# Kernel optimization log

Hardware: AMD Instinct MI355X
Metric: run time of the kernel (lower is better)

Reference implementation:

```python
import jax, jax.numpy as jnp
import numpy as np

B, NEG = 2, 16            # queries, negatives per query
N, E, D = 10000, 80000, 128  # nodes, edges, feature dim (in_dim == out_dim)
NUM_REL = 237
L = 3                     # PNA layers
NODE_RATIO = 0.1
K = max(1, int(NODE_RATIO * N))  # static top-k: every repeated graph has exactly N nodes
EPS = 1e-5


def _score(hidden, rel, lin_W, lin_b, m1_W, m1_b, m2_W, m2_b):
    heur = jnp.concatenate([hidden, rel], axis=-1) @ lin_W + lin_b
    x = heur * hidden
    h = jax.nn.relu(x @ m1_W + m1_b)
    return jnp.squeeze(h @ m2_W + m2_b, -1)


def _pna_conv(hidden, src, dst, emask, deg, pre_W, pre_b, post_W, post_b, out_W, out_b):
    """PNA layer with mean/max/min/std aggregators and identity/amplification/attenuation
    scalers, restricted to edges where emask is True. deg is the (clamped >=1) degree used
    by the scalers."""
    BN = hidden.shape[0]
    # message: pre-linear on [x_i (target), x_j (source)] per edge  -> (Erep, D)
    m = jnp.concatenate([hidden[dst], hidden[src]], axis=-1) @ pre_W + pre_b
    w = emask.astype(hidden.dtype)[:, None]
    cnt = jax.ops.segment_sum(emask.astype(hidden.dtype), dst, num_segments=BN)
    denom = jnp.maximum(cnt, 1.0)[:, None]
    s1 = jax.ops.segment_sum(m * w, dst, num_segments=BN)
    s2 = jax.ops.segment_sum(m * m * w, dst, num_segments=BN)
    mean = s1 / denom
    var = jax.nn.relu(s2 / denom - mean * mean)
    std = jnp.sqrt(var + EPS)
    has = (cnt > 0)[:, None]
    mx = jnp.where(has, jax.ops.segment_max(jnp.where(emask[:, None], m, -jnp.inf), dst, num_segments=BN), 0.0)
    mn = jnp.where(has, jax.ops.segment_min(jnp.where(emask[:, None], m, jnp.inf), dst, num_segments=BN), 0.0)
    agg = jnp.concatenate([mean, mx, mn, std], axis=-1)           # (BN, 4D)
    logd = jnp.log(deg + 1.0)                                     # deg >= 1 -> logd > 0
    avg_log = jnp.mean(logd)
    agg = jnp.concatenate([agg, agg * (logd / avg_log)[:, None], agg * (avg_log / logd)[:, None]], axis=-1)  # (BN, 12D)
    return (agg @ post_W + post_b) @ out_W + out_b


def _forward(h_index, r_index, t_index, hidden_states, edge_index, rel_embedding,
             lin_W, lin_b, m1_W, m1_b, m2_W, m2_b, pre_W, pre_b, post_W, post_b, out_W, out_b):
    sc = (lin_W, lin_b, m1_W, m1_b, m2_W, m2_b)
    # negative_sample_to_tail
    is_t_neg = jnp.all(h_index == h_index[:, :1], axis=-1, keepdims=True)
    h_idx = jnp.where(is_t_neg, h_index, t_index)
    t_idx = jnp.where(is_t_neg, t_index, h_index)
    r_idx = jnp.where(is_t_neg, r_index, r_index + NUM_REL)
    # repeat_graph
    offsets = jnp.arange(B, dtype=h_idx.dtype) * N               # (B,)
    src = jnp.tile(edge_index[0], B) + jnp.repeat(offsets, E)    # (B*E,)
    dst = jnp.tile(edge_index[1], B) + jnp.repeat(offsets, E)
    BN = B * N
    rel_embeds = rel_embedding[r_idx[:, 0]].astype(hidden_states.dtype)  # (B, D)
    flat_h = h_idx[:, 0] + offsets
    flat_t = t_idx[:, 0] + offsets
    # literal `repeat_interleave(N, dim=0)[:B]` quirk -> row arange(B)//N of gathered embs
    sel = jnp.arange(B) // N
    h_vals = hidden_states[h_idx[:, 0]][sel]                     # (B, D)
    t_vals = hidden_states[t_idx[:, 0]][sel]
    # init_input_embeds: boundary condition + initial score at head nodes
    boundary = jnp.zeros((BN, D), hidden_states.dtype).at[flat_t].set(t_vals).at[flat_h].set(h_vals)
    score = jnp.zeros(BN, jnp.float32).at[flat_h].set(_score(h_vals, rel_embeds, *sc))
    hidden = boundary
    rel_per_node = jnp.repeat(rel_embeds, N, axis=0)             # (BN, D), rel_embeds[batch_rep]
    rows = jnp.arange(B)[:, None]
    for l in range(L):
        # select_edges_pyg with degree_ratio=1.0: all out-edges of per-graph top-k nodes
        _, idx = jax.lax.top_k(score.reshape(B, N), K)           # (B, K)
        node_sel = jnp.zeros((B, N), bool).at[rows, idx].set(True).reshape(-1)
        emask = node_sel[src]                                    # (B*E,) selected-edge mask
        out_deg = jax.ops.segment_sum(emask.astype(jnp.float32), src, num_segments=BN)
        deg_sub = jnp.maximum(out_deg.astype(hidden.dtype), 1.0)
        new_hidden = _pna_conv(hidden, src, dst, emask, deg_sub,
                               pre_W[l], pre_b[l], post_W[l], post_b[l], out_W[l], out_b[l])
        # residual only for nodes with selected outgoing edges
        hidden = jnp.where((out_deg > 0)[:, None], hidden + new_hidden, hidden)
        score = _score(hidden, rel_per_node, *sc)
    # read out scores at (repeated) tail indices -> (B, NEG)
    return score[t_idx + offsets[:, None]]


def setup_inputs() -> dict:
    key = jax.random.key(0)
    ks = jax.random.split(key, 14)
    s = 0.05
    hi = jax.random.randint(ks[0], (B, 1), 0, N)
    h_index = jnp.tile(hi, (1, NEG))                 # constant per row (assert in forward)
    r0 = jax.random.randint(ks[1], (B, 1), 0, NUM_REL)
    r_index = jnp.tile(r0, (1, NEG))                 # constant per row (assert in forward)
    t_index = jax.random.randint(ks[2], (B, NEG), 0, N)
    hidden_states = jax.random.normal(ks[3], (N, D), jnp.float32)
    edge_index = jax.random.randint(ks[4], (2, E), 0, N)
    return {
        "h_index": h_index, "r_index": r_index, "t_index": t_index,
        "hidden_states": hidden_states, "edge_index": edge_index,
        "rel_embedding": jax.random.normal(ks[5], (2 * NUM_REL, D), jnp.float32) * s,
        "lin_W": jax.random.normal(ks[6], (2 * D, D), jnp.float32) * s, "lin_b": jnp.zeros(D, jnp.float32),
        "m1_W": jax.random.normal(ks[7], (D, D), jnp.float32) * s, "m1_b": jnp.zeros(D, jnp.float32),
        "m2_W": jax.random.normal(ks[8], (D, 1), jnp.float32) * s, "m2_b": jnp.zeros(1, jnp.float32),
        "pre_W": jax.random.normal(ks[9], (L, 2 * D, D), jnp.float32) * s, "pre_b": jnp.zeros((L, D), jnp.float32),
        "post_W": jax.random.normal(ks[10], (L, 12 * D, D), jnp.float32) * s, "post_b": jnp.zeros((L, D), jnp.float32),
        "out_W": jax.random.normal(ks[11], (L, D, D), jnp.float32) * s, "out_b": jnp.zeros((L, D), jnp.float32),
    }


def reference(h_index, r_index, t_index, hidden_states, edge_index, rel_embedding,
              lin_W, lin_b, m1_W, m1_b, m2_W, m2_b, pre_W, pre_b, post_W, post_b, out_W, out_b):
    return _forward(h_index, r_index, t_index, hidden_states, edge_index, rel_embedding,
                    lin_W, lin_b, m1_W, m1_b, m2_W, m2_b, pre_W, pre_b, post_W, post_b, out_W, out_b)
```

## Files before the change

### kernel.cpp

```cpp
#include <hip/hip_runtime.h>
#include <math.h>

#define Bq 2
#define NEG 16
#define Nn 10000
#define Ee 80000
#define Dd 128
#define NUM_REL 237
#define Ll 3
#define K_SEL 1000
#define BN (Bq*Nn)
#define EPSV 1e-5f
#define MAXACT 2048
#define MAXTOUCH 8192
#define SELCAP 3328
#define LN2F 0.69314718056f

constexpr size_t HID_OFF   = 0;
constexpr size_t SCORE_OFF = HID_OFF   + (size_t)BN*Dd*4;
constexpr size_t CVEC_OFF  = SCORE_OFF + (size_t)BN*4;
constexpr size_t HDR_OFF   = CVEC_OFF  + (size_t)Bq*Dd*4;
constexpr size_t THR_OFF   = HDR_OFF   + 64*4;
constexpr size_t SEL_OFF   = THR_OFF   + Bq*8;
constexpr size_t DEG_OFF   = SEL_OFF   + (size_t)BN*4;
constexpr size_t SLOT_OFF  = DEG_OFF   + (size_t)BN*4;
constexpr size_t CNT_OFF   = SLOT_OFF  + (size_t)BN*4;
constexpr size_t SDEG_OFF  = CNT_OFF   + (size_t)MAXACT*4;
constexpr size_t S1_OFF    = SDEG_OFF  + (size_t)MAXACT*4;
constexpr size_t S2_OFF    = S1_OFF    + (size_t)MAXACT*Dd*4;
constexpr size_t MXB_OFF   = S2_OFF    + (size_t)MAXACT*Dd*4;
constexpr size_t MNB_OFF   = MXB_OFF   + (size_t)MAXACT*Dd*4;
constexpr size_t TPART_OFF = MNB_OFF   + (size_t)MAXACT*Dd*4;
constexpr size_t ALIST_OFF = TPART_OFF + (size_t)4*MAXACT*Dd*4;
constexpr size_t FLAG_OFF  = ALIST_OFF + (size_t)MAXACT*4;
constexpr size_t TLIST_OFF = FLAG_OFF  + (size_t)BN*4;
constexpr size_t EDGE_OFF  = TLIST_OFF + (size_t)MAXTOUCH*4;
constexpr size_t CTR_OFF   = EDGE_OFF  + (size_t)Bq*Ee*2*4;

__device__ __forceinline__ unsigned encf(float f){
  unsigned u = __float_as_uint(f);
  return (u & 0x80000000u) ? ~u : (u | 0x80000000u);
}
__device__ __forceinline__ float decf(unsigned e){
  unsigned u = (e & 0x80000000u) ? (e & 0x7FFFFFFFu) : ~e;
  return __uint_as_float(u);
}
__device__ __forceinline__ unsigned long long make_key(float f, int i){
  unsigned d = ~encf(f);
  return ((unsigned long long)d << 32) | (unsigned)i;
}

__global__ void k_zero(float* hidden, unsigned* flag){
  int i = blockIdx.x*blockDim.x + threadIdx.x;
  if (i < BN*Dd/4) ((float4*)hidden)[i] = make_float4(0.f,0.f,0.f,0.f);
  if (i < BN) flag[i] = 0u;
}

__global__ __launch_bounds__(256) void k_prep(
    const int* h_index, const int* r_index, const int* t_index,
    const float* hidden_states, const float* rel_embedding,
    const float* lin_W, const float* lin_b, const float* m1_W, const float* m1_b,
    const float* m2_W, const float* m2_b,
    int* hdr, float* cvec, float* hidden, float* score,
    unsigned* flag, int* tlist, unsigned* ctr){
  __shared__ int sh_fh[Bq], sh_ft[Bq], sh_r0[Bq], sh_hsrc, sh_tsrc;
  __shared__ float s_relv[Bq][Dd], s_cvec[Bq][Dd], s_hv[Dd], s_x[Bq][Dd], s_p[Bq][Dd];
  __shared__ float s_s0[Dd];
  __shared__ float sc0_sh;
  int tid = threadIdx.x;
  if (tid == 0){
    int n = 0;
    for (int b=0;b<Bq;b++){
      bool eq = true;
      for (int j=1;j<NEG;j++) eq = eq && (h_index[b*NEG+j]==h_index[b*NEG]);
      int h0 = eq ? h_index[b*NEG] : t_index[b*NEG];
      int t0 = eq ? t_index[b*NEG] : h_index[b*NEG];
      int r0 = eq ? r_index[b*NEG] : r_index[b*NEG] + NUM_REL;
      sh_fh[b] = h0 + b*Nn; sh_ft[b] = t0 + b*Nn; sh_r0[b] = r0;
      hdr[0+b] = sh_fh[b]; hdr[2+b] = sh_ft[b];
      for (int j=0;j<NEG;j++){
        int tj = eq ? t_index[b*NEG+j] : h_index[b*NEG+j];
        hdr[4 + b*NEG + j] = tj + b*Nn;
      }
      if (b==0){ sh_hsrc = h0; sh_tsrc = t0; }
      if (!flag[sh_ft[b]]){ flag[sh_ft[b]] = 1u; tlist[n++] = sh_ft[b]; }
      if (!flag[sh_fh[b]]){ flag[sh_fh[b]] = 1u; tlist[n++] = sh_fh[b]; }
    }
    ctr[3] = (unsigned)n;
  }
  __syncthreads();
  int b = tid >> 7, d = tid & 127;
  s_relv[b][d] = rel_embedding[(size_t)sh_r0[b]*Dd + d];
  if (b == 0){
    s_hv[d] = hidden_states[(size_t)sh_hsrc*Dd + d];
    s_s0[d] = fmaxf(m1_b[d], 0.f) * m2_W[d];
  }
  __syncthreads();
  if (tid == 0){
    float s = m2_b[0];
    for (int k=0;k<Dd;k++) s += s_s0[k];
    sc0_sh = s;
    ctr[4] = __float_as_uint(s);
  }
  float acc = lin_b[d];
  #pragma unroll 8
  for (int k=0;k<Dd;k++) acc += s_relv[b][k]*lin_W[(Dd+k)*Dd + d];
  s_cvec[b][d] = acc; cvec[b*Dd+d] = acc;
  hidden[(size_t)sh_ft[b]*Dd + d] = hidden_states[(size_t)sh_tsrc*Dd + d];
  hidden[(size_t)sh_fh[b]*Dd + d] = hidden_states[(size_t)sh_hsrc*Dd + d];
  __syncthreads();
  float sc0 = sc0_sh;
  for (int i = tid; i < BN; i += 256) score[i] = sc0;
  float hv = s_hv[d];
  float heur = s_cvec[b][d];
  #pragma unroll 8
  for (int k=0;k<Dd;k++) heur += s_hv[k]*lin_W[k*Dd + d];
  s_x[b][d] = heur * hv;
  __syncthreads();
  float a2 = m1_b[d];
  #pragma unroll 8
  for (int k=0;k<Dd;k++) a2 += s_x[b][k]*m1_W[k*Dd + d];
  s_p[b][d] = fmaxf(a2, 0.f) * m2_W[d];
  __syncthreads();
  if (tid < Bq){
    float s = m2_b[0];
    for (int k=0;k<Dd;k++) s += s_p[tid][k];
    score[sh_fh[tid]] = s;
  }
}

__global__ __launch_bounds__(256) void k_select(
    const float* score, const int* tlist, const unsigned* ctr,
    unsigned long long* thr){
  int b = blockIdx.x;
  int nt = (int)ctr[3];
  unsigned d0 = ~encf(__uint_as_float(ctr[4]));
  __shared__ unsigned sd[SELCAP];
  __shared__ unsigned short sidx[SELCAP];
  __shared__ unsigned hist[256], histT[256];
  __shared__ int ntb_sh;
  __shared__ unsigned long long pref_sh;
  __shared__ unsigned kk_sh;
  int tid = threadIdx.x;
  if (tid==0){ ntb_sh = 0; pref_sh = 0ull; kk_sh = K_SEL; }
  __syncthreads();
  int vlo = b*Nn, vhi = vlo + Nn;
  for (int i = tid; i < nt; i += 256){
    int v = tlist[i];
    if (v >= vlo && v < vhi){
      int pos = atomicAdd(&ntb_sh, 1);
      if (pos < SELCAP){
        sd[pos] = ~encf(score[v]);
        sidx[pos] = (unsigned short)(v - vlo);
      }
    }
  }
  __syncthreads();
  int ntb = min(ntb_sh, SELCAP);
  unsigned nvirt = (unsigned)(Nn - ntb);
  for (int pass = 7; pass >= 0; --pass){
    hist[tid] = 0u; histT[tid] = 0u;
    __syncthreads();
    unsigned long long pref = pref_sh;
    int sh_hi = 8*(pass+1);
    for (int j = tid; j < ntb; j += 256){
      unsigned long long key = ((unsigned long long)sd[j] << 32) | (unsigned long long)sidx[j];
      bool ok = (pass==7) || ((key >> sh_hi) == (pref >> sh_hi));
      if (ok) atomicAdd(&hist[(unsigned)(key >> (8*pass)) & 255u], 1u);
      if (pass < 4){
        unsigned idx = sidx[j];
        bool oki = (pass == 3) || ((idx >> sh_hi) == (((unsigned)pref) >> sh_hi));
        if (oki) atomicAdd(&histT[(idx >> (8*pass)) & 255u], 1u);
      }
    }
    __syncthreads();
    if (pass >= 4){
      if (tid == 0){
        unsigned long long keyv_hi = ((unsigned long long)d0 << 32);
        bool ok = (pass==7) || ((keyv_hi >> sh_hi) == (pref >> sh_hi));
        if (ok) atomicAdd(&hist[(d0 >> (8*(pass-4))) & 255u], nvirt);
      }
    } else {
      if ((unsigned)(pref >> 32) == d0){
        unsigned long long hf = 0ull;
        if (pass < 3) hf = (unsigned long long)((((unsigned)pref) >> sh_hi)) << sh_hi;
        unsigned long long lo = hf + ((unsigned long long)tid << (8*pass));
        unsigned long long hi = lo + (1ull << (8*pass));
        unsigned long long nn = (unsigned long long)Nn;
        unsigned long long l2 = lo < nn ? lo : nn;
        unsigned long long h2 = hi < nn ? hi : nn;
        if (h2 > l2){
          unsigned c = (unsigned)(h2 - l2) - histT[tid];
          if (c > 0u) atomicAdd(&hist[tid], c);
        }
      }
    }
    __syncthreads();
    if (tid < 256){
      unsigned kk = kk_sh;
      unsigned cum = 0;
      for (int i=0;i<tid;i++) cum += hist[i];
      unsigned h = hist[tid];
      if (h > 0u && cum < kk && kk <= cum + h){
        pref_sh |= ((unsigned long long)tid) << (8*pass);
        kk_sh = kk - cum;
      }
    }
    __syncthreads();
  }
  if (tid==0) thr[b] = pref_sh;
}

__global__ void k_mask(const float* score, const unsigned long long* thr, unsigned* sel,
                       unsigned* out_deg, float* s1, float* s2,
                       unsigned* mxb, unsigned* mnb, unsigned* cnt, unsigned* ctr){
  int i = blockIdx.x*blockDim.x + threadIdx.x;
  if (i < BN){
    int b = i / Nn; int v = i - b*Nn;
    sel[i] = (make_key(score[i], v) <= thr[b]) ? 1u : 0u;
    out_deg[i] = 0u;
  }
  if (i < MAXACT*Dd){ s1[i]=0.f; s2[i]=0.f; mxb[i]=0u; mnb[i]=0xFFFFFFFFu; }
  if (i < MAXACT) cnt[i]=0u;
  if (i < 3) ctr[i]=0u;
}

__global__ void k_degree(const int* ei, const unsigned* sel, unsigned* out_deg){
  int e = blockIdx.x*blockDim.x + threadIdx.x;
  if (e >= Ee) return;
  int s0 = ei[e];
  #pragma unroll
  for (int b=0;b<Bq;b++){
    int v = s0 + b*Nn;
    if (sel[v]) atomicAdd(&out_deg[v], 1u);
  }
}

__global__ void k_active(const unsigned* out_deg, int* node_slot, int* alist,
                         float* slot_deg, unsigned* ctr, unsigned* flag, int* tlist){
  int v = blockIdx.x*blockDim.x + threadIdx.x;
  if (v >= BN) return;
  unsigned dg = out_deg[v];
  if (dg > 0u){
    int slot = (int)atomicAdd(&ctr[0], 1u);
    alist[slot] = v; node_slot[v] = slot; slot_deg[slot] = (float)dg;
    atomicAdd((float*)&ctr[2], logf((float)dg + 1.0f));
    if (atomicExch(&flag[v], 1u) == 0u){
      int p = (int)atomicAdd(&ctr[3], 1u);
      tlist[p] = v;
    }
  }
}

__global__ void k_edges(const int* ei, const unsigned* sel, const unsigned* out_deg,
                        const int* node_slot, int* edges, unsigned* cnt, unsigned* ctr){
  int e = blockIdx.x*blockDim.x + threadIdx.x;
  if (e >= Ee) return;
  int s0 = ei[e], d0 = ei[Ee + e];
  #pragma unroll
  for (int b=0;b<Bq;b++){
    int s = s0 + b*Nn, dv = d0 + b*Nn;
    if (sel[s] && out_deg[dv] > 0u){
      int slot = node_slot[dv];
      int j = (int)atomicAdd(&ctr[1], 1u);
      edges[2*j] = s; edges[2*j+1] = slot;
      atomicAdd(&cnt[slot], 1u);
    }
  }
}

__global__ __launch_bounds__(128) void k_messages(
    const float* hidden, const int* edges, const int* alist,
    const float* preW, const float* preb,
    float* s1, float* s2, unsigned* mxb, unsigned* mnb, const unsigned* ctr){
  int ne = (int)ctr[1];
  int tid = threadIdx.x;
  __shared__ float sd[4][Dd], ss[4][Dd];
  __shared__ int dsl[4];
  float pb = preb[tid];
  for (int j0 = blockIdx.x*4; j0 < ne; j0 += gridDim.x*4){
    int nv = ne - j0; if (nv > 4) nv = 4;
    if (tid < 4){
      int j = j0 + ((tid < nv) ? tid : 0);
      dsl[tid] = edges[2*j+1];
    }
    #pragma unroll
    for (int e=0;e<4;e++){
      int j = j0 + ((e < nv) ? e : 0);
      int s = edges[2*j];
      int dv = alist[edges[2*j+1]];
      sd[e][tid] = hidden[(size_t)dv*Dd + tid];
      ss[e][tid] = hidden[(size_t)s*Dd + tid];
    }
    __syncthreads();
    float a[4] = {pb, pb, pb, pb};
    #pragma unroll 4
    for (int k=0;k<Dd;k++){
      float w0 = preW[k*Dd + tid];
      float w1 = preW[(Dd+k)*Dd + tid];
      #pragma unroll
      for (int e=0;e<4;e++) a[e] += sd[e][k]*w0 + ss[e][k]*w1;
    }
    for (int e=0;e<nv;e++){
      int dslot = dsl[e];
      atomicAdd(&s1[dslot*Dd + tid], a[e]);
      atomicAdd(&s2[dslot*Dd + tid], a[e]*a[e]);
      atomicMax(&mxb[dslot*Dd + tid], encf(a[e]));
      atomicMin(&mnb[dslot*Dd + tid], encf(a[e]));
    }
    __syncthreads();
  }
}

__global__ __launch_bounds__(512) void k_post(
    const unsigned* cnt, const float* s1, const float* s2,
    const unsigned* mxb, const unsigned* mnb, const float* slot_deg,
    const float* postW, float* tpart, const unsigned* ctr){
  int na = (int)ctr[0];
  int bid = blockIdx.x;
  int tile = bid & 63, ch = bid >> 6;
  if (tile*32 >= na) return;
  float logsum = __uint_as_float(ctr[2]);
  float avg = (logsum + (float)(BN - na)*LN2F) / (float)BN;
  __shared__ float lb[32*136];
  __shared__ float wbuf[3*16*128];
  __shared__ float sden[32];
  __shared__ unsigned shas[32];
  int tid = threadIdx.x;
  if (tid < 32){
    unsigned c = cnt[tile*32 + tid];
    sden[tid] = fmaxf((float)c, 1.0f);
    shas[tid] = c;
  }
  __syncthreads();
  for (int idx = tid; idx < 32*Dd; idx += 512){
    int sl = idx >> 7, kk = idx & 127;
    int gi = (tile*32 + sl)*Dd + kk;
    float den = sden[sl];
    float val;
    if (ch == 0)      val = s1[gi]/den;
    else if (ch == 1) val = shas[sl] ? decf(mxb[gi]) : 0.f;
    else if (ch == 2) val = shas[sl] ? decf(mnb[gi]) : 0.f;
    else {
      float mv = s1[gi]/den;
      float var = s2[gi]/den - mv*mv;
      val = sqrtf(fmaxf(var, 0.f) + EPSV);
    }
    lb[sl*136 + kk] = val;
  }
  int cg = tid & 31, rg = tid >> 5;
  int c0 = cg*4;
  float a0[2][4], a1[2][4], a2[2][4];
  #pragma unroll
  for (int i=0;i<2;i++)
    #pragma unroll
    for (int j=0;j<4;j++){ a0[i][j]=0.f; a1[i][j]=0.f; a2[i][j]=0.f; }
  for (int chunk = 0; chunk < 8; ++chunk){
    #pragma unroll
    for (int i = 0; i < 3; ++i){
      int f = tid + i*512;
      int q = f >> 9, r = f & 511;
      int kk = r >> 5, c4 = r & 31;
      int grow = q*512 + ch*128 + chunk*16 + kk;
      ((float4*)wbuf)[f] = *(const float4*)(postW + (size_t)grow*Dd + c4*4);
    }
    __syncthreads();
    #pragma unroll
    for (int k4 = 0; k4 < 4; ++k4){
      float4 av0 = *(const float4*)&lb[(rg*2+0)*136 + chunk*16 + k4*4];
      float4 av1 = *(const float4*)&lb[(rg*2+1)*136 + chunk*16 + k4*4];
      #pragma unroll
      for (int j = 0; j < 4; ++j){
        int kk = k4*4 + j;
        float4 w0 = *(const float4*)&wbuf[kk*128 + c0];
        float4 w1 = *(const float4*)&wbuf[(16+kk)*128 + c0];
        float4 w2 = *(const float4*)&wbuf[(32+kk)*128 + c0];
        float av[2] = { (&av0.x)[j], (&av1.x)[j] };
        #pragma unroll
        for (int i=0;i<2;i++){
          float a = av[i];
          a0[i][0] += a*w0.x; a0[i][1] += a*w0.y; a0[i][2] += a*w0.z; a0[i][3] += a*w0.w;
          a1[i][0] += a*w1.x; a1[i][1] += a*w1.y; a1[i][2] += a*w1.z; a1[i][3] += a*w1.w;
          a2[i][0] += a*w2.x; a2[i][1] += a*w2.y; a2[i][2] += a*w2.z; a2[i][3] += a*w2.w;
        }
      }
    }
    __syncthreads();
  }
  #pragma unroll
  for (int i=0;i<2;i++){
    int slot = tile*32 + rg*2 + i;
    if (slot < na){
      float dg = slot_deg[slot];
      float logd = logf(dg + 1.f);
      float al = logd/avg, be = avg/logd;
      float4 r;
      r.x = a0[i][0] + al*a1[i][0] + be*a2[i][0];
      r.y = a0[i][1] + al*a1[i][1] + be*a2[i][1];
      r.z = a0[i][2] + al*a1[i][2] + be*a2[i][2];
      r.w = a0[i][3] + al*a1[i][3] + be*a2[i][3];
      *(float4*)(tpart + (size_t)ch*MAXACT*Dd + (size_t)slot*Dd + c0) = r;
    }
  }
}

__global__ __launch_bounds__(256) void k_out_resid(
    const float* tpart, const int* alist, const float* outW, const float* outb,
    const float* postb, float* hidden, const unsigned* ctr){
  int na = (int)ctr[0];
  int tile = blockIdx.x;
  if (tile*32 >= na) return;
  __shared__ float tr[32*136];
  __shared__ float wbuf[16*128];
  int tid = threadIdx.x;
  for (int idx = tid; idx < 32*Dd; idx += 256){
    int sl = idx >> 7, kk = idx & 127;
    size_t o = (size_t)(tile*32 + sl)*Dd + kk;
    tr[sl*136 + kk] = tpart[o] + tpart[(size_t)MAXACT*Dd + o]
                    + tpart[(size_t)2*MAXACT*Dd + o] + tpart[(size_t)3*MAXACT*Dd + o]
                    + postb[kk];
  }
  int cg = tid & 31, rg = tid >> 5;
  int c0 = cg*4;
  float4 ob = *(const float4*)(outb + c0);
  float acc[4][4];
  #pragma unroll
  for (int r=0;r<4;r++){ acc[r][0]=ob.x; acc[r][1]=ob.y; acc[r][2]=ob.z; acc[r][3]=ob.w; }
  for (int chunk = 0; chunk < 8; ++chunk){
    #pragma unroll
    for (int i = 0; i < 2; ++i){
      int f = tid + i*256;
      int kk = f >> 5, c4 = f & 31;
      ((float4*)wbuf)[f] = *(const float4*)(outW + (size_t)(chunk*16 + kk)*Dd + c4*4);
    }
    __syncthreads();
    #pragma unroll
    for (int k4 = 0; k4 < 4; ++k4){
      float4 av[4];
      #pragma unroll
      for (int r=0;r<4;r++)
        av[r] = *(const float4*)&tr[(rg*4+r)*136 + chunk*16 + k4*4];
      #pragma unroll
      for (int j = 0; j < 4; ++j){
        float4 w = *(const float4*)&wbuf[(k4*4+j)*128 + c0];
        #pragma unroll
        for (int r=0;r<4;r++){
          float a = (&av[r].x)[j];
          acc[r][0] += a*w.x; acc[r][1] += a*w.y; acc[r][2] += a*w.z; acc[r][3] += a*w.w;
        }
      }
    }
    __syncthreads();
  }
  #pragma unroll
  for (int r=0;r<4;r++){
    int slot = tile*32 + rg*4 + r;
    if (slot < na){
      int v = alist[slot];
      float* hp = hidden + (size_t)v*Dd + c0;
      float4 h4 = *(float4*)hp;
      h4.x += acc[r][0]; h4.y += acc[r][1]; h4.z += acc[r][2]; h4.w += acc[r][3];
      *(float4*)hp = h4;
    }
  }
}

__global__ __launch_bounds__(256) void k_score(
    const float* hidden, const float* cvec, const float* linW,
    const float* m1W, const float* m1b, const float* m2W, const float* m2b,
    const int* tlist, const unsigned* ctr, float* score,
    const int* ovr, int ovr_n){
  int nt = (ovr_n > 0) ? ovr_n : (int)ctr[3];
  const int* list = (ovr_n > 0) ? ovr : tlist;
  int nb = blockIdx.x * 32;
  if (nb >= nt) return;
  __shared__ float sh[32*Dd];
  __shared__ float sx[32*Dd];
  __shared__ float sc[2*Dd];
  __shared__ int   sv[32];
  __shared__ float red[32*33];
  int tid = threadIdx.x;
  if (tid < 32){
    int idx = nb + tid;
    sv[tid] = (idx < nt) ? list[idx] : list[nb];
  }
  sc[tid] = cvec[tid];
  __syncthreads();
  for (int q = tid; q < 32*32; q += 256){
    int row = q >> 5, f4 = q & 31;
    ((float4*)sh)[row*32 + f4] = ((const float4*)(hidden + (size_t)sv[row]*Dd))[f4];
  }
  __syncthreads();
  int cg = tid & 31, rg = tid >> 5;
  int c0 = cg*4;
  float acc[4][4];
  #pragma unroll
  for (int i=0;i<4;i++){ acc[i][0]=0.f; acc[i][1]=0.f; acc[i][2]=0.f; acc[i][3]=0.f; }
  for (int k4=0;k4<32;k4++){
    float4 av[4];
    #pragma unroll
    for (int i=0;i<4;i++) av[i] = ((float4*)sh)[(rg*4+i)*32 + k4];
    #pragma unroll
    for (int j=0;j<4;j++){
      float4 w = *(const float4*)(linW + (size_t)(k4*4+j)*Dd + c0);
      #pragma unroll
      for (int i=0;i<4;i++){
        float a = (&av[i].x)[j];
        acc[i][0] += a*w.x; acc[i][1] += a*w.y; acc[i][2] += a*w.z; acc[i][3] += a*w.w;
      }
    }
  }
  #pragma unroll
  for (int i=0;i<4;i++){
    int row = rg*4 + i;
    int bb = (sv[row] >= Nn) ? 1 : 0;
    float4 cv = *(float4*)&sc[bb*Dd + c0];
    float4 hv = ((float4*)sh)[row*32 + cg];
    float4 x;
    x.x = (acc[i][0] + cv.x)*hv.x;
    x.y = (acc[i][1] + cv.y)*hv.y;
    x.z = (acc[i][2] + cv.z)*hv.z;
    x.w = (acc[i][3] + cv.w)*hv.w;
    ((float4*)sx)[row*32 + cg] = x;
  }
  __syncthreads();
  #pragma unroll
  for (int i=0;i<4;i++){ acc[i][0]=0.f; acc[i][1]=0.f; acc[i][2]=0.f; acc[i][3]=0.f; }
  for (int k4=0;k4<32;k4++){
    float4 av[4];
    #pragma unroll
    for (int i=0;i<4;i++) av[i] = ((float4*)sx)[(rg*4+i)*32 + k4];
    #pragma unroll
    for (int j=0;j<4;j++){
      float4 w = *(const float4*)(m1W + (size_t)(k4*4+j)*Dd + c0);
      #pragma unroll
      for (int i=0;i<4;i++){
        float a = (&av[i].x)[j];
        acc[i][0] += a*w.x; acc[i][1] += a*w.y; acc[i][2] += a*w.z; acc[i][3] += a*w.w;
      }
    }
  }
  float4 mb = *(const float4*)(m1b + c0);
  float4 mw = *(const float4*)(m2W + c0);
  #pragma unroll
  for (int i=0;i<4;i++){
    float p0 = fmaxf(acc[i][0]+mb.x, 0.f)*mw.x;
    float p1 = fmaxf(acc[i][1]+mb.y, 0.f)*mw.y;
    float p2 = fmaxf(acc[i][2]+mb.z, 0.f)*mw.z;
    float p3 = fmaxf(acc[i][3]+mb.w, 0.f)*mw.w;
    red[(rg*4+i)*33 + cg] = p0+p1+p2+p3;
  }
  __syncthreads();
  if (tid < 32){
    float s = m2b[0];
    for (int g=0; g<32; g++) s += red[tid*33 + g];
    if (nb + tid < nt) score[sv[tid]] = s;
  }
}

__global__ void k_gather(const float* score, const int* hdr, float* out){
  int i = threadIdx.x;
  if (i < Bq*NEG) out[i] = score[hdr[4+i]];
}

extern "C" void kernel_launch(void* const* d_in, const int* in_sizes, int n_in,
                              void* d_out, int out_size, void* d_ws, size_t ws_size,
                              hipStream_t stream){
  const int*   h_index       = (const int*)d_in[0];
  const int*   r_index       = (const int*)d_in[1];
  const int*   t_index       = (const int*)d_in[2];
  const float* hidden_states = (const float*)d_in[3];
  const int*   edge_index    = (const int*)d_in[4];
  const float* rel_embedding = (const float*)d_in[5];
  const float* lin_W  = (const float*)d_in[6];
  const float* lin_b  = (const float*)d_in[7];
  const float* m1_W   = (const float*)d_in[8];
  const float* m1_b   = (const float*)d_in[9];
  const float* m2_W   = (const float*)d_in[10];
  const float* m2_b   = (const float*)d_in[11];
  const float* pre_W  = (const float*)d_in[12];
  const float* pre_b  = (const float*)d_in[13];
  const float* post_W = (const float*)d_in[14];
  const float* post_b = (const float*)d_in[15];
  const float* out_W  = (const float*)d_in[16];
  const float* out_b  = (const float*)d_in[17];

  char* ws = (char*)d_ws;
  float*    hidden   = (float*)(ws + HID_OFF);
  float*    score    = (float*)(ws + SCORE_OFF);
  float*    cvec     = (float*)(ws + CVEC_OFF);
  int*      hdr      = (int*)(ws + HDR_OFF);
  unsigned long long* thr = (unsigned long long*)(ws + THR_OFF);
  unsigned* sel      = (unsigned*)(ws + SEL_OFF);
  unsigned* out_deg  = (unsigned*)(ws + DEG_OFF);
  int*      node_slot= (int*)(ws + SLOT_OFF);
  unsigned* cnt      = (unsigned*)(ws + CNT_OFF);
  float*    slot_deg = (float*)(ws + SDEG_OFF);
  float*    s1       = (float*)(ws + S1_OFF);
  float*    s2       = (float*)(ws + S2_OFF);
  unsigned* mxb      = (unsigned*)(ws + MXB_OFF);
  unsigned* mnb      = (unsigned*)(ws + MNB_OFF);
  float*    tpart    = (float*)(ws + TPART_OFF);
  int*      alist    = (int*)(ws + ALIST_OFF);
  unsigned* flag     = (unsigned*)(ws + FLAG_OFF);
  int*      tlist    = (int*)(ws + TLIST_OFF);
  int*      edges    = (int*)(ws + EDGE_OFF);
  unsigned* ctr      = (unsigned*)(ws + CTR_OFF);

  k_zero<<<(BN*Dd/4 + 255)/256, 256, 0, stream>>>(hidden, flag);
  k_prep<<<1, 256, 0, stream>>>(h_index, r_index, t_index, hidden_states, rel_embedding,
                                lin_W, lin_b, m1_W, m1_b, m2_W, m2_b,
                                hdr, cvec, hidden, score, flag, tlist, ctr);
  for (int l = 0; l < Ll; ++l){
    const float* preWl  = pre_W  + (size_t)l*2*Dd*Dd;
    const float* prebl  = pre_b  + (size_t)l*Dd;
    const float* postWl = post_W + (size_t)l*12*Dd*Dd;
    const float* postbl = post_b + (size_t)l*Dd;
    const float* outWl  = out_W  + (size_t)l*Dd*Dd;
    const float* outbl  = out_b  + (size_t)l*Dd;

    k_select<<<Bq, 256, 0, stream>>>(score, tlist, ctr, thr);
    k_mask<<<(MAXACT*Dd + 255)/256, 256, 0, stream>>>(score, thr, sel, out_deg,
                                                      s1, s2, mxb, mnb, cnt, ctr);
    k_degree<<<(Ee + 255)/256, 256, 0, stream>>>(edge_index, sel, out_deg);
    k_active<<<(BN + 255)/256, 256, 0, stream>>>(out_deg, node_slot, alist, slot_deg,
                                                 ctr, flag, tlist);
    k_edges<<<(Ee + 255)/256, 256, 0, stream>>>(edge_index, sel, out_deg, node_slot,
                                                edges, cnt, ctr);
    k_messages<<<512, 128, 0, stream>>>(hidden, edges, alist, preWl, prebl,
                                        s1, s2, mxb, mnb, ctr);
    k_post<<<256, 512, 0, stream>>>(cnt, s1, s2, mxb, mnb, slot_deg, postWl, tpart, ctr);
    k_out_resid<<<MAXACT/32, 256, 0, stream>>>(tpart, alist, outWl, outbl, postbl,
                                               hidden, ctr);
    if (l < Ll-1){
      k_score<<<MAXTOUCH/32, 256, 0, stream>>>(hidden, cvec, lin_W, m1_W, m1_b, m2_W, m2_b,
                                               tlist, ctr, score, tlist, 0);
    } else {
      k_score<<<1, 256, 0, stream>>>(hidden, cvec, lin_W, m1_W, m1_b, m2_W, m2_b,
                                     tlist, ctr, score, hdr + 4, Bq*NEG);
    }
  }
  k_gather<<<1, 64, 0, stream>>>(score, hdr, (float*)d_out);
}
```

Before: 481.7 us.

## Fuse init, selection+zeroing, mask into degree, edge filtering into messages

Measured after the change: 538.6 us. +11.8%, slower.

```diff
diff --git a/kernel.cpp b/kernel.cpp
--- a/kernel.cpp
+++ b/kernel.cpp
@@ -21,8 +21,7 @@
 constexpr size_t CVEC_OFF  = SCORE_OFF + (size_t)BN*4;
 constexpr size_t HDR_OFF   = CVEC_OFF  + (size_t)Bq*Dd*4;
 constexpr size_t THR_OFF   = HDR_OFF   + 64*4;
-constexpr size_t SEL_OFF   = THR_OFF   + Bq*8;
-constexpr size_t DEG_OFF   = SEL_OFF   + (size_t)BN*4;
+constexpr size_t DEG_OFF   = THR_OFF   + 64*8;
 constexpr size_t SLOT_OFF  = DEG_OFF   + (size_t)BN*4;
 constexpr size_t CNT_OFF   = SLOT_OFF  + (size_t)BN*4;
 constexpr size_t SDEG_OFF  = CNT_OFF   + (size_t)MAXACT*4;
@@ -50,89 +49,121 @@
   return ((unsigned long long)d << 32) | (unsigned)i;
 }
 
-__global__ void k_zero(float* hidden, unsigned* flag){
-  int i = blockIdx.x*blockDim.x + threadIdx.x;
-  if (i < BN*Dd/4) ((float4*)hidden)[i] = make_float4(0.f,0.f,0.f,0.f);
-  if (i < BN) flag[i] = 0u;
-}
-
-__global__ __launch_bounds__(256) void k_prep(
+__global__ __launch_bounds__(256) void k_init(
     const int* h_index, const int* r_index, const int* t_index,
     const float* hidden_states, const float* rel_embedding,
     const float* lin_W, const float* lin_b, const float* m1_W, const float* m1_b,
     const float* m2_W, const float* m2_b,
     int* hdr, float* cvec, float* hidden, float* score,
     unsigned* flag, int* tlist, unsigned* ctr){
-  __shared__ int sh_fh[Bq], sh_ft[Bq], sh_r0[Bq], sh_hsrc, sh_tsrc;
-  __shared__ float s_relv[Bq][Dd], s_cvec[Bq][Dd], s_hv[Dd], s_x[Bq][Dd], s_p[Bq][Dd];
-  __shared__ float s_s0[Dd];
-  __shared__ float sc0_sh;
+  __shared__ int sfh[Bq], sft[Bq], sr0[Bq], shsrc, stsrc;
+  __shared__ float sp[Dd];
+  __shared__ float ssc0;
+  __shared__ float relv[Bq][Dd], cvv[Bq][Dd], hv[Dd], xx[Bq][Dd], pp[Bq][Dd];
   int tid = threadIdx.x;
   if (tid == 0){
-    int n = 0;
     for (int b=0;b<Bq;b++){
       bool eq = true;
       for (int j=1;j<NEG;j++) eq = eq && (h_index[b*NEG+j]==h_index[b*NEG]);
       int h0 = eq ? h_index[b*NEG] : t_index[b*NEG];
       int t0 = eq ? t_index[b*NEG] : h_index[b*NEG];
       int r0 = eq ? r_index[b*NEG] : r_index[b*NEG] + NUM_REL;
-      sh_fh[b] = h0 + b*Nn; sh_ft[b] = t0 + b*Nn; sh_r0[b] = r0;
-      hdr[0+b] = sh_fh[b]; hdr[2+b] = sh_ft[b];
-      for (int j=0;j<NEG;j++){
-        int tj = eq ? t_index[b*NEG+j] : h_index[b*NEG+j];
-        hdr[4 + b*NEG + j] = tj + b*Nn;
-      }
-      if (b==0){ sh_hsrc = h0; sh_tsrc = t0; }
-      if (!flag[sh_ft[b]]){ flag[sh_ft[b]] = 1u; tlist[n++] = sh_ft[b]; }
-      if (!flag[sh_fh[b]]){ flag[sh_fh[b]] = 1u; tlist[n++] = sh_fh[b]; }
-    }
-    ctr[3] = (unsigned)n;
-  }
-  __syncthreads();
-  int b = tid >> 7, d = tid & 127;
-  s_relv[b][d] = rel_embedding[(size_t)sh_r0[b]*Dd + d];
-  if (b == 0){
-    s_hv[d] = hidden_states[(size_t)sh_hsrc*Dd + d];
-    s_s0[d] = fmaxf(m1_b[d], 0.f) * m2_W[d];
-  }
+      sfh[b] = h0 + b*Nn; sft[b] = t0 + b*Nn; sr0[b] = r0;
+      if (b==0){ shsrc = h0; stsrc = t0; }
+    }
+  }
+  if (tid < Dd) sp[tid] = fmaxf(m1_b[tid], 0.f) * m2_W[tid];
   __syncthreads();
   if (tid == 0){
     float s = m2_b[0];
-    for (int k=0;k<Dd;k++) s += s_s0[k];
-    sc0_sh = s;
-    ctr[4] = __float_as_uint(s);
-  }
-  float acc = lin_b[d];
-  #pragma unroll 8
-  for (int k=0;k<Dd;k++) acc += s_relv[b][k]*lin_W[(Dd+k)*Dd + d];
-  s_cvec[b][d] = acc; cvec[b*Dd+d] = acc;
-  hidden[(size_t)sh_ft[b]*Dd + d] = hidden_states[(size_t)sh_tsrc*Dd + d];
-  hidden[(size_t)sh_fh[b]*Dd + d] = hidden_states[(size_t)sh_hsrc*Dd + d];
-  __syncthreads();
-  float sc0 = sc0_sh;
-  for (int i = tid; i < BN; i += 256) score[i] = sc0;
-  float hv = s_hv[d];
-  float heur = s_cvec[b][d];
-  #pragma unroll 8
-  for (int k=0;k<Dd;k++) heur += s_hv[k]*lin_W[k*Dd + d];
-  s_x[b][d] = heur * hv;
-  __syncthreads();
-  float a2 = m1_b[d];
-  #pragma unroll 8
-  for (int k=0;k<Dd;k++) a2 += s_x[b][k]*m1_W[k*Dd + d];
-  s_p[b][d] = fmaxf(a2, 0.f) * m2_W[d];
-  __syncthreads();
-  if (tid < Bq){
-    float s = m2_b[0];
-    for (int k=0;k<Dd;k++) s += s_p[tid][k];
-    score[sh_fh[tid]] = s;
-  }
-}
-
-__global__ __launch_bounds__(256) void k_select(
-    const float* score, const int* tlist, const unsigned* ctr,
-    unsigned long long* thr){
-  int b = blockIdx.x;
+    for (int k=0;k<Dd;k++) s += sp[k];
+    ssc0 = s;
+  }
+  __syncthreads();
+  float sc0 = ssc0;
+  int fh0 = sfh[0], fh1 = sfh[1], ft0 = sft[0], ft1 = sft[1];
+  int gth = blockIdx.x*256 + tid, gstr = gridDim.x*256;
+  for (int i = gth; i < BN*Dd/4; i += gstr){
+    int row = i >> 5, c4 = i & 31;
+    float4 v;
+    if (row == fh0 || row == fh1)
+      v = ((const float4*)(hidden_states + (size_t)shsrc*Dd))[c4];
+    else if (row == ft0 || row == ft1)
+      v = ((const float4*)(hidden_states + (size_t)stsrc*Dd))[c4];
+    else v = make_float4(0.f,0.f,0.f,0.f);
+    ((float4*)hidden)[i] = v;
+  }
+  for (int i = gth; i < BN; i += gstr){
+    flag[i] = (i==fh0 || i==fh1 || i==ft0 || i==ft1) ? 1u : 0u;
+    if (i != fh0 && i != fh1) score[i] = sc0;
+  }
+  if (blockIdx.x == 0){
+    if (tid == 0){
+      int tl[4]; int n = 0;
+      for (int b=0;b<Bq;b++){
+        hdr[b] = sfh[b]; hdr[2+b] = sft[b];
+        bool eq = true;
+        for (int j=1;j<NEG;j++) eq = eq && (h_index[b*NEG+j]==h_index[b*NEG]);
+        for (int j=0;j<NEG;j++){
+          int tj = eq ? t_index[b*NEG+j] : h_index[b*NEG+j];
+          hdr[4 + b*NEG + j] = tj + b*Nn;
+        }
+        int c1 = sft[b]; bool f1=false;
+        for (int q=0;q<n;q++) f1 = f1 || (tl[q]==c1);
+        if (!f1) tl[n++] = c1;
+        int c2 = sfh[b]; bool f2=false;
+        for (int q=0;q<n;q++) f2 = f2 || (tl[q]==c2);
+        if (!f2) tl[n++] = c2;
+      }
+      for (int q=0;q<n;q++) tlist[q] = tl[q];
+      ctr[3] = (unsigned)n;
+      ctr[4] = __float_as_uint(sc0);
+    }
+    int b = tid >> 7, d = tid & 127;
+    relv[b][d] = rel_embedding[(size_t)sr0[b]*Dd + d];
+    if (b == 0) hv[d] = hidden_states[(size_t)shsrc*Dd + d];
+    __syncthreads();
+    float acc = lin_b[d];
+    #pragma unroll 8
+    for (int k=0;k<Dd;k++) acc += relv[b][k]*lin_W[(Dd+k)*Dd + d];
+    cvv[b][d] = acc; cvec[b*Dd+d] = acc;
+    float heur = acc;
+    #pragma unroll 8
+    for (int k=0;k<Dd;k++) heur += hv[k]*lin_W[k*Dd + d];
+    xx[b][d] = heur * hv[d];
+    __syncthreads();
+    float a2 = m1_b[d];
+    #pragma unroll 8
+    for (int k=0;k<Dd;k++) a2 += xx[b][k]*m1_W[k*Dd + d];
+    pp[b][d] = fmaxf(a2, 0.f) * m2_W[d];
+    __syncthreads();
+    if (tid < Bq){
+      float s = m2_b[0];
+      for (int k=0;k<Dd;k++) s += pp[tid][k];
+      score[sfh[tid]] = s;
+    }
+  }
+}
+
+__global__ __launch_bounds__(256) void k_selz(
+    const float* score, const int* tlist, unsigned* ctr, unsigned long long* thr,
+    unsigned* out_deg, float* s1, float* s2, unsigned* mxb, unsigned* mnb, unsigned* cnt){
+  int bid = blockIdx.x, tid = threadIdx.x;
+  if (bid >= 2){
+    int z0 = (bid-2)*256 + tid, zstr = (gridDim.x-2)*256;
+    float4 z4 = make_float4(0.f,0.f,0.f,0.f);
+    uint4 zi = make_uint4(0u,0u,0u,0u);
+    uint4 fi = make_uint4(~0u,~0u,~0u,~0u);
+    for (int i=z0; i<MAXACT*Dd/4; i+=zstr){
+      ((float4*)s1)[i]=z4; ((float4*)s2)[i]=z4;
+      ((uint4*)mxb)[i]=zi; ((uint4*)mnb)[i]=fi;
+    }
+    for (int i=z0; i<BN; i+=zstr) out_deg[i]=0u;
+    for (int i=z0; i<MAXACT; i+=zstr) cnt[i]=0u;
+    if (bid==2 && tid<3) ctr[tid]=0u;
+    return;
+  }
+  int b = bid;
   int nt = (int)ctr[3];
   unsigned d0 = ~encf(__uint_as_float(ctr[4]));
   __shared__ unsigned sd[SELCAP];
@@ -141,7 +172,6 @@
   __shared__ int ntb_sh;
   __shared__ unsigned long long pref_sh;
   __shared__ unsigned kk_sh;
-  int tid = threadIdx.x;
   if (tid==0){ ntb_sh = 0; pref_sh = 0ull; kk_sh = K_SEL; }
   __syncthreads();
   int vlo = b*Nn, vhi = vlo + Nn;
@@ -211,28 +241,22 @@
   if (tid==0) thr[b] = pref_sh;
 }
 
-__global__ void k_mask(const float* score, const unsigned long long* thr, unsigned* sel,
-                       unsigned* out_deg, float* s1, float* s2,
-                       unsigned* mxb, unsigned* mnb, unsigned* cnt, unsigned* ctr){
-  int i = blockIdx.x*blockDim.x + threadIdx.x;
-  if (i < BN){
-    int b = i / Nn; int v = i - b*Nn;
-    sel[i] = (make_key(score[i], v) <= thr[b]) ? 1u : 0u;
-    out_deg[i] = 0u;
-  }
-  if (i < MAXACT*Dd){ s1[i]=0.f; s2[i]=0.f; mxb[i]=0u; mnb[i]=0xFFFFFFFFu; }
-  if (i < MAXACT) cnt[i]=0u;
-  if (i < 3) ctr[i]=0u;
-}
-
-__global__ void k_degree(const int* ei, const unsigned* sel, unsigned* out_deg){
+__global__ void k_degree(const int* ei, const float* score, const unsigned long long* thr,
+                         unsigned* out_deg, int* sedges, unsigned* ctr){
   int e = blockIdx.x*blockDim.x + threadIdx.x;
   if (e >= Ee) return;
-  int s0 = ei[e];
-  #pragma unroll
-  for (int b=0;b<Bq;b++){
-    int v = s0 + b*Nn;
-    if (sel[v]) atomicAdd(&out_deg[v], 1u);
+  unsigned long long th0 = thr[0], th1 = thr[1];
+  int s0 = ei[e], d0 = ei[Ee + e];
+  if (make_key(score[s0], s0) <= th0){
+    atomicAdd(&out_deg[s0], 1u);
+    int j = (int)atomicAdd(&ctr[1], 1u);
+    sedges[2*j] = s0; sedges[2*j+1] = d0;
+  }
+  int s1v = s0 + Nn, d1v = d0 + Nn;
+  if (make_key(score[s1v], s0) <= th1){
+    atomicAdd(&out_deg[s1v], 1u);
+    int j = (int)atomicAdd(&ctr[1], 1u);
+    sedges[2*j] = s1v; sedges[2*j+1] = d1v;
   }
 }
 
@@ -252,63 +276,64 @@
   }
 }
 
-__global__ void k_edges(const int* ei, const unsigned* sel, const unsigned* out_deg,
-                        const int* node_slot, int* edges, unsigned* cnt, unsigned* ctr){
-  int e = blockIdx.x*blockDim.x + threadIdx.x;
-  if (e >= Ee) return;
-  int s0 = ei[e], d0 = ei[Ee + e];
-  #pragma unroll
-  for (int b=0;b<Bq;b++){
-    int s = s0 + b*Nn, dv = d0 + b*Nn;
-    if (sel[s] && out_deg[dv] > 0u){
-      int slot = node_slot[dv];
-      int j = (int)atomicAdd(&ctr[1], 1u);
-      edges[2*j] = s; edges[2*j+1] = slot;
-      atomicAdd(&cnt[slot], 1u);
-    }
-  }
-}
-
+#define MSG_GRID 512
 __global__ __launch_bounds__(128) void k_messages(
-    const float* hidden, const int* edges, const int* alist,
+    const float* hidden, const int* sedges, const int* node_slot, const unsigned* out_deg,
     const float* preW, const float* preb,
-    float* s1, float* s2, unsigned* mxb, unsigned* mnb, const unsigned* ctr){
-  int ne = (int)ctr[1];
+    float* s1, float* s2, unsigned* mxb, unsigned* mnb, unsigned* cnt, const unsigned* ctr){
+  int ns = (int)ctr[1];
   int tid = threadIdx.x;
-  __shared__ float sd[4][Dd], ss[4][Dd];
+  int bid = blockIdx.x;
+  __shared__ int qs[128], qd[128], qsl[128];
+  __shared__ int qn_sh;
+  __shared__ float sdl[4][Dd], ssl[4][Dd];
   __shared__ int dsl[4];
   float pb = preb[tid];
-  for (int j0 = blockIdx.x*4; j0 < ne; j0 += gridDim.x*4){
-    int nv = ne - j0; if (nv > 4) nv = 4;
-    if (tid < 4){
-      int j = j0 + ((tid < nv) ? tid : 0);
-      dsl[tid] = edges[2*j+1];
-    }
-    #pragma unroll
-    for (int e=0;e<4;e++){
-      int j = j0 + ((e < nv) ? e : 0);
-      int s = edges[2*j];
-      int dv = alist[edges[2*j+1]];
-      sd[e][tid] = hidden[(size_t)dv*Dd + tid];
-      ss[e][tid] = hidden[(size_t)s*Dd + tid];
-    }
-    __syncthreads();
-    float a[4] = {pb, pb, pb, pb};
-    #pragma unroll 4
-    for (int k=0;k<Dd;k++){
-      float w0 = preW[k*Dd + tid];
-      float w1 = preW[(Dd+k)*Dd + tid];
+  int kmax = (ns - bid + MSG_GRID - 1) / MSG_GRID;
+  if (bid >= ns) kmax = 0;
+  for (int k0 = 0; k0 < kmax; k0 += 128){
+    if (tid == 0) qn_sh = 0;
+    __syncthreads();
+    int k = k0 + tid;
+    if (k < kmax){
+      int j = bid + k*MSG_GRID;
+      int dv = sedges[2*j+1];
+      if (out_deg[dv] > 0u){
+        int slot = node_slot[dv];
+        int p = atomicAdd(&qn_sh, 1);
+        qs[p] = sedges[2*j]; qd[p] = dv; qsl[p] = slot;
+        atomicAdd(&cnt[slot], 1u);
+      }
+    }
+    __syncthreads();
+    int nq = qn_sh;
+    for (int q0 = 0; q0 < nq; q0 += 4){
+      int nv = nq - q0; if (nv > 4) nv = 4;
+      if (tid < 4) dsl[tid] = qsl[q0 + ((tid < nv) ? tid : 0)];
       #pragma unroll
-      for (int e=0;e<4;e++) a[e] += sd[e][k]*w0 + ss[e][k]*w1;
-    }
-    for (int e=0;e<nv;e++){
-      int dslot = dsl[e];
-      atomicAdd(&s1[dslot*Dd + tid], a[e]);
-      atomicAdd(&s2[dslot*Dd + tid], a[e]*a[e]);
-      atomicMax(&mxb[dslot*Dd + tid], encf(a[e]));
-      atomicMin(&mnb[dslot*Dd + tid], encf(a[e]));
-    }
-    __syncthreads();
+      for (int e2=0;e2<4;e2++){
+        int qq = q0 + ((e2 < nv) ? e2 : 0);
+        sdl[e2][tid] = hidden[(size_t)qd[qq]*Dd + tid];
+        ssl[e2][tid] = hidden[(size_t)qs[qq]*Dd + tid];
+      }
+      __syncthreads();
+      float a[4] = {pb, pb, pb, pb};
+      #pragma unroll 4
+      for (int kk=0;kk<Dd;kk++){
+        float w0 = preW[kk*Dd + tid];
+        float w1 = preW[(Dd+kk)*Dd + tid];
+        #pragma unroll
+        for (int e2=0;e2<4;e2++) a[e2] += sdl[e2][kk]*w0 + ssl[e2][kk]*w1;
+      }
+      for (int e2=0;e2<nv;e2++){
+        int dslot = dsl[e2];
+        atomicAdd(&s1[dslot*Dd + tid], a[e2]);
+        atomicAdd(&s2[dslot*Dd + tid], a[e2]*a[e2]);
+        atomicMax(&mxb[dslot*Dd + tid], encf(a[e2]));
+        atomicMin(&mnb[dslot*Dd + tid], encf(a[e2]));
+      }
+      __syncthreads();
+    }
   }
 }
 
@@ -469,7 +494,7 @@
     const float* hidden, const float* cvec, const float* linW,
     const float* m1W, const float* m1b, const float* m2W, const float* m2b,
     const int* tlist, const unsigned* ctr, float* score,
-    const int* ovr, int ovr_n){
+    const int* ovr, int ovr_n, float* outdest){
   int nt = (ovr_n > 0) ? ovr_n : (int)ctr[3];
   const int* list = (ovr_n > 0) ? ovr : tlist;
   int nb = blockIdx.x * 32;
@@ -554,13 +579,11 @@
   if (tid < 32){
     float s = m2b[0];
     for (int g=0; g<32; g++) s += red[tid*33 + g];
-    if (nb + tid < nt) score[sv[tid]] = s;
-  }
-}
-
-__global__ void k_gather(const float* score, const int* hdr, float* out){
-  int i = threadIdx.x;
-  if (i < Bq*NEG) out[i] = score[hdr[4+i]];
+    if (nb + tid < nt){
+      if (outdest) outdest[nb + tid] = s;
+      else         score[sv[tid]] = s;
+    }
+  }
 }
 
 extern "C" void kernel_launch(void* const* d_in, const int* in_sizes, int n_in,
@@ -591,7 +614,6 @@
   float*    cvec     = (float*)(ws + CVEC_OFF);
   int*      hdr      = (int*)(ws + HDR_OFF);
   unsigned long long* thr = (unsigned long long*)(ws + THR_OFF);
-  unsigned* sel      = (unsigned*)(ws + SEL_OFF);
   unsigned* out_deg  = (unsigned*)(ws + DEG_OFF);
   int*      node_slot= (int*)(ws + SLOT_OFF);
   unsigned* cnt      = (unsigned*)(ws + CNT_OFF);
@@ -604,13 +626,12 @@
   int*      alist    = (int*)(ws + ALIST_OFF);
   unsigned* flag     = (unsigned*)(ws + FLAG_OFF);
   int*      tlist    = (int*)(ws + TLIST_OFF);
-  int*      edges    = (int*)(ws + EDGE_OFF);
+  int*      sedges   = (int*)(ws + EDGE_OFF);
   unsigned* ctr      = (unsigned*)(ws + CTR_OFF);
 
-  k_zero<<<(BN*Dd/4 + 255)/256, 256, 0, stream>>>(hidden, flag);
-  k_prep<<<1, 256, 0, stream>>>(h_index, r_index, t_index, hidden_states, rel_embedding,
-                                lin_W, lin_b, m1_W, m1_b, m2_W, m2_b,
-                                hdr, cvec, hidden, score, flag, tlist, ctr);
+  k_init<<<2048, 256, 0, stream>>>(h_index, r_index, t_index, hidden_states, rel_embedding,
+                                   lin_W, lin_b, m1_W, m1_b, m2_W, m2_b,
+                                   hdr, cvec, hidden, score, flag, tlist, ctr);
   for (int l = 0; l < Ll; ++l){
     const float* preWl  = pre_W  + (size_t)l*2*Dd*Dd;
     const float* prebl  = pre_b  + (size_t)l*Dd;
@@ -619,26 +640,21 @@
     const float* outWl  = out_W  + (size_t)l*Dd*Dd;
     const float* outbl  = out_b  + (size_t)l*Dd;
 
-    k_select<<<Bq, 256, 0, stream>>>(score, tlist, ctr, thr);
-    k_mask<<<(MAXACT*Dd + 255)/256, 256, 0, stream>>>(score, thr, sel, out_deg,
-                                                      s1, s2, mxb, mnb, cnt, ctr);
-    k_degree<<<(Ee + 255)/256, 256, 0, stream>>>(edge_index, sel, out_deg);
+    k_selz<<<512, 256, 0, stream>>>(score, tlist, ctr, thr, out_deg, s1, s2, mxb, mnb, cnt);
+    k_degree<<<(Ee + 255)/256, 256, 0, stream>>>(edge_index, score, thr, out_deg, sedges, ctr);
     k_active<<<(BN + 255)/256, 256, 0, stream>>>(out_deg, node_slot, alist, slot_deg,
                                                  ctr, flag, tlist);
-    k_edges<<<(Ee + 255)/256, 256, 0, stream>>>(edge_index, sel, out_deg, node_slot,
-                                                edges, cnt, ctr);
-    k_messages<<<512, 128, 0, stream>>>(hidden, edges, alist, preWl, prebl,
-                                        s1, s2, mxb, mnb, ctr);
+    k_messages<<<MSG_GRID, 128, 0, stream>>>(hidden, sedges, node_slot, out_deg,
+                                             preWl, prebl, s1, s2, mxb, mnb, cnt, ctr);
     k_post<<<256, 512, 0, stream>>>(cnt, s1, s2, mxb, mnb, slot_deg, postWl, tpart, ctr);
     k_out_resid<<<MAXACT/32, 256, 0, stream>>>(tpart, alist, outWl, outbl, postbl,
                                                hidden, ctr);
     if (l < Ll-1){
       k_score<<<MAXTOUCH/32, 256, 0, stream>>>(hidden, cvec, lin_W, m1_W, m1_b, m2_W, m2_b,
-                                               tlist, ctr, score, tlist, 0);
+                                               tlist, ctr, score, tlist, 0, nullptr);
     } else {
       k_score<<<1, 256, 0, stream>>>(hidden, cvec, lin_W, m1_W, m1_b, m2_W, m2_b,
-                                     tlist, ctr, score, hdr + 4, Bq*NEG);
-    }
-  }
-  k_gather<<<1, 64, 0, stream>>>(score, hdr, (float*)d_out);
-}
+                                     tlist, ctr, score, hdr + 4, Bq*NEG, (float*)d_out);
+    }
+  }
+}
```
